# Kernel optimization log

Hardware: AMD Instinct MI355X
Metric: run time of the kernel (lower is better)

Reference implementation:

```python
import jax, jax.numpy as jnp
import numpy as np
import math

B, L, D, K = 16, 8192, 256, 320
BN_EPS = 1e-5


def setup_inputs() -> dict:
    key = jax.random.key(0)
    k1, k2, k3, k4 = jax.random.split(key, 4)
    x = jax.random.normal(k1, (B, L, D), dtype=jnp.float32)
    bn_weight = 1.0 + 0.1 * jax.random.normal(k2, (D,), dtype=jnp.float32)
    bn_bias = 0.1 * jax.random.normal(k3, (D,), dtype=jnp.float32)
    # xavier_uniform for Embedding(numCodes, codeDim)
    a = math.sqrt(6.0 / (K + D))
    codebook = jax.random.uniform(k4, (K, D), minval=-a, maxval=a, dtype=jnp.float32)
    return {"x": x, "bn_weight": bn_weight, "bn_bias": bn_bias, "codebook": codebook}


def batchnorm1d(x, weight, bias):
    # BatchNorm1d in training mode: stats over (batch, length) per channel,
    # biased variance for normalization (matches torch).
    mean = jnp.mean(x, axis=(0, 1))
    var = jnp.var(x, axis=(0, 1))
    return (x - mean) * jax.lax.rsqrt(var + BN_EPS) * weight + bias


def reference(x, bn_weight, bn_bias, codebook):
    xb = batchnorm1d(x, bn_weight, bn_bias)            # [B, L, D]
    flat = xb.reshape(-1, D)                           # [B*L, D]
    # squared euclidean distance (same argmin as torch.cdist)
    d2 = (jnp.sum(flat * flat, axis=-1, keepdims=True)
          - 2.0 * flat @ codebook.T
          + jnp.sum(codebook * codebook, axis=-1))     # [B*L, K]
    indices = jnp.argmin(d2, axis=-1)                  # [B*L]
    codes = codebook[indices].reshape(B, L, D)         # gather nearest codes
    return codes, indices.reshape(B, L, 1)
```

## Files before the change

### kernel.cpp

```cpp
#include <hip/hip_runtime.h>
#include <hip/hip_bf16.h>

#define NROW 131072
#define D 256
#define K 320
#define BN_EPS 1e-5f
#define FIXSCALE 16777216.0f

typedef _Float16 half8 __attribute__((ext_vector_type(8)));
typedef float f32x4 __attribute__((ext_vector_type(4)));


__global__ __launch_bounds__(256) void k_zero(unsigned long long* __restrict__ acc) {
  acc[threadIdx.x] = 0ull;
  acc[256 + threadIdx.x] = 0ull;
}

__global__ __launch_bounds__(256) void k_stats_partial(const float* __restrict__ x,
                                                       unsigned long long* __restrict__ acc) {
  const int d = threadIdx.x;
  const int blk = blockIdx.x;
  const float* p = x + (size_t)blk * 256 * D + d;
  float s = 0.f, q = 0.f;
  #pragma unroll 4
  for (int r = 0; r < 256; ++r) {
    float v = p[(size_t)r * D];
    s += v;
    q = fmaf(v, v, q);
  }
  long long si = llrintf(s * FIXSCALE);
  long long qi = llrintf(q * FIXSCALE);
  atomicAdd(&acc[d],       (unsigned long long)si);
  atomicAdd(&acc[256 + d], (unsigned long long)qi);
}

__global__ __launch_bounds__(256) void k_stats_final(const unsigned long long* __restrict__ acc,
                                                     const float* __restrict__ cb,
                                                     float* __restrict__ meanb,
                                                     float* __restrict__ rsb,
                                                     float* __restrict__ cnorm) {
  const int t = threadIdx.x;
  if (blockIdx.x == 0) {
    double s = (double)(long long)acc[t]       / (double)FIXSCALE;
    double q = (double)(long long)acc[256 + t] / (double)FIXSCALE;
    double mean = s / (double)NROW;
    double var  = q / (double)NROW - mean * mean;
    meanb[t] = (float)mean;
    rsb[t]   = (float)(1.0 / sqrt(var + (double)BN_EPS));
  } else {
    for (int code = t; code < K; code += 256) {
      const float* c = cb + (size_t)code * D;
      float s = 0.f;
      for (int dd = 0; dd < D; ++dd) s = fmaf(c[dd], c[dd], s);
      cnorm[code] = s;
    }
  }
}

__global__ __launch_bounds__(64) void k_cbprep(const float* __restrict__ cb,
                                               _Float16* __restrict__ cbx) {
  const int nt = blockIdx.x;
  const int ks = blockIdx.y;
  const int l  = threadIdx.x;
  const int code = nt * 16 + (l & 15);
  const int d0 = ks * 32 + (l >> 4) * 8;
  const float* src = cb + (size_t)code * D + d0;
  const size_t bh = ((size_t)(nt * 2 + 0) * 8 + ks) * 512 + l * 8;
  const size_t bl = ((size_t)(nt * 2 + 1) * 8 + ks) * 512 + l * 8;
  #pragma unroll
  for (int j = 0; j < 8; ++j) {
    float v = src[j];
    _Float16 h = (_Float16)v;
    _Float16 lo = (_Float16)(v - (float)h);
    cbx[bh + j] = h;
    cbx[bl + j] = lo;
  }
}

__global__ __launch_bounds__(512) void k_main(const float* __restrict__ x,
                                              const float* __restrict__ w,
                                              const float* __restrict__ bias,
                                              const float* __restrict__ cb,
                                              const float* __restrict__ meanb,
                                              const float* __restrict__ rsb,
                                              const float* __restrict__ cnorm,
                                              const _Float16* __restrict__ cbx,
                                              float* __restrict__ out) {
  __shared__ _Float16 Bbuf[2][16384];
  __shared__ float sxs[256];
  __shared__ int bsel[256];

  const int t = threadIdx.x;
  const int lane = t & 63;
  const int wv = t >> 6;
  const int c15 = lane & 15;
  const int g = lane >> 4;
  const int row0 = (int)blockIdx.x * 256;

  float4 s0, s1, s2, s3;
  const char* stg_src = (const char*)cbx + (size_t)t * 16;
#define ISSUE(c) {                                                  \
    const char* p_ = stg_src + (size_t)(c) * 32768;                 \
    s0 = *(const float4*)(p_);                                      \
    s1 = *(const float4*)(p_ + 8192);                               \
    s2 = *(const float4*)(p_ + 16384);                              \
    s3 = *(const float4*)(p_ + 24576);                              \
  }
#define WRITE(b) {                                                  \
    char* q_ = (char*)Bbuf[b] + t * 16;                             \
    *(float4*)(q_)         = s0;                                    \
    *(float4*)(q_ + 8192)  = s1;                                    \
    *(float4*)(q_ + 16384) = s2;                                    \
    *(float4*)(q_ + 24576) = s3;                                    \
  }

  ISSUE(0);

  half8 ah[2][8], al[2][8];
  float accq0 = 0.f, accq1 = 0.f;
  {
    const int dbase = g * 8;
    const float* xp0 = x + (size_t)(row0 + wv * 32 + c15) * D + dbase;
    const float* xp1 = x + (size_t)(row0 + wv * 32 + 16 + c15) * D + dbase;
    #pragma unroll
    for (int ks = 0; ks < 8; ++ks) {
      const int d0 = dbase + ks * 32;
      float4 m0 = *(const float4*)(meanb + d0);
      float4 m1 = *(const float4*)(meanb + d0 + 4);
      float4 r0 = *(const float4*)(rsb + d0);
      float4 r1 = *(const float4*)(rsb + d0 + 4);
      float4 w0 = *(const float4*)(w + d0);
      float4 w1 = *(const float4*)(w + d0 + 4);
      float4 b0 = *(const float4*)(bias + d0);
      float4 b1 = *(const float4*)(bias + d0 + 4);
      {
        float4 xa = *(const float4*)(xp0 + ks * 32);
        float4 xb2 = *(const float4*)(xp0 + ks * 32 + 4);
        float o0 = ((xa.x - m0.x) * r0.x) * w0.x + b0.x;
        float o1 = ((xa.y - m0.y) * r0.y) * w0.y + b0.y;
        float o2 = ((xa.z - m0.z) * r0.z) * w0.z + b0.z;
        float o3 = ((xa.w - m0.w) * r0.w) * w0.w + b0.w;
        float o4 = ((xb2.x - m1.x) * r1.x) * w1.x + b1.x;
        float o5 = ((xb2.y - m1.y) * r1.y) * w1.y + b1.y;
        float o6 = ((xb2.z - m1.z) * r1.z) * w1.z + b1.z;
        float o7 = ((xb2.w - m1.w) * r1.w) * w1.w + b1.w;
        accq0 = fmaf(o0, o0, accq0); accq0 = fmaf(o1, o1, accq0);
        accq0 = fmaf(o2, o2, accq0); accq0 = fmaf(o3, o3, accq0);
        accq0 = fmaf(o4, o4, accq0); accq0 = fmaf(o5, o5, accq0);
        accq0 = fmaf(o6, o6, accq0); accq0 = fmaf(o7, o7, accq0);
        _Float16 h;
        h = (_Float16)o0; ah[0][ks][0] = h; al[0][ks][0] = (_Float16)(o0 - (float)h);
        h = (_Float16)o1; ah[0][ks][1] = h; al[0][ks][1] = (_Float16)(o1 - (float)h);
        h = (_Float16)o2; ah[0][ks][2] = h; al[0][ks][2] = (_Float16)(o2 - (float)h);
        h = (_Float16)o3; ah[0][ks][3] = h; al[0][ks][3] = (_Float16)(o3 - (float)h);
        h = (_Float16)o4; ah[0][ks][4] = h; al[0][ks][4] = (_Float16)(o4 - (float)h);
        h = (_Float16)o5; ah[0][ks][5] = h; al[0][ks][5] = (_Float16)(o5 - (float)h);
        h = (_Float16)o6; ah[0][ks][6] = h; al[0][ks][6] = (_Float16)(o6 - (float)h);
        h = (_Float16)o7; ah[0][ks][7] = h; al[0][ks][7] = (_Float16)(o7 - (float)h);
      }
      {
        float4 xa = *(const float4*)(xp1 + ks * 32);
        float4 xb2 = *(const float4*)(xp1 + ks * 32 + 4);
        float o0 = ((xa.x - m0.x) * r0.x) * w0.x + b0.x;
        float o1 = ((xa.y - m0.y) * r0.y) * w0.y + b0.y;
        float o2 = ((xa.z - m0.z) * r0.z) * w0.z + b0.z;
        float o3 = ((xa.w - m0.w) * r0.w) * w0.w + b0.w;
        float o4 = ((xb2.x - m1.x) * r1.x) * w1.x + b1.x;
        float o5 = ((xb2.y - m1.y) * r1.y) * w1.y + b1.y;
        float o6 = ((xb2.z - m1.z) * r1.z) * w1.z + b1.z;
        float o7 = ((xb2.w - m1.w) * r1.w) * w1.w + b1.w;
        accq1 = fmaf(o0, o0, accq1); accq1 = fmaf(o1, o1, accq1);
        accq1 = fmaf(o2, o2, accq1); accq1 = fmaf(o3, o3, accq1);
        accq1 = fmaf(o4, o4, accq1); accq1 = fmaf(o5, o5, accq1);
        accq1 = fmaf(o6, o6, accq1); accq1 = fmaf(o7, o7, accq1);
        _Float16 h;
        h = (_Float16)o0; ah[1][ks][0] = h; al[1][ks][0] = (_Float16)(o0 - (float)h);
        h = (_Float16)o1; ah[1][ks][1] = h; al[1][ks][1] = (_Float16)(o1 - (float)h);
        h = (_Float16)o2; ah[1][ks][2] = h; al[1][ks][2] = (_Float16)(o2 - (float)h);
        h = (_Float16)o3; ah[1][ks][3] = h; al[1][ks][3] = (_Float16)(o3 - (float)h);
        h = (_Float16)o4; ah[1][ks][4] = h; al[1][ks][4] = (_Float16)(o4 - (float)h);
        h = (_Float16)o5; ah[1][ks][5] = h; al[1][ks][5] = (_Float16)(o5 - (float)h);
        h = (_Float16)o6; ah[1][ks][6] = h; al[1][ks][6] = (_Float16)(o6 - (float)h);
        h = (_Float16)o7; ah[1][ks][7] = h; al[1][ks][7] = (_Float16)(o7 - (float)h);
      }
    }
  }
  {
    float v0 = accq0 + __shfl_xor(accq0, 16);
    float sx0 = v0 + __shfl_xor(v0, 32);
    float v1 = accq1 + __shfl_xor(accq1, 16);
    float sx1 = v1 + __shfl_xor(v1, 32);
    if (lane < 16) {
      sxs[wv * 32 + lane]      = sx0;
      sxs[wv * 32 + 16 + lane] = sx1;
    }
  }

  WRITE(0);
  ISSUE(1);
  __syncthreads();

  float bv[2][4];
  int   bix[2][4];
  #pragma unroll
  for (int i = 0; i < 2; ++i)
    #pragma unroll
    for (int r = 0; r < 4; ++r) { bv[i][r] = 3.4e38f; bix[i][r] = 0x7fffffff; }

  float sxr[2][4];
  #pragma unroll
  for (int i = 0; i < 2; ++i)
    #pragma unroll
    for (int r = 0; r < 4; ++r) sxr[i][r] = sxs[wv * 32 + i * 16 + g * 4 + r];

  for (int c = 0; c < 10; ++c) {
    if (c + 1 < 10) WRITE((c + 1) & 1);
    if (c + 2 < 10) ISSUE(c + 2);

    const _Float16* bb = Bbuf[c & 1] + lane * 8;
    f32x4 acc[2][2];
    #pragma unroll
    for (int i = 0; i < 2; ++i)
      #pragma unroll
      for (int tt = 0; tt < 2; ++tt) acc[i][tt] = (f32x4){0.f, 0.f, 0.f, 0.f};

    #pragma unroll
    for (int tt = 0; tt < 2; ++tt) {
      #pragma unroll
      for (int ks = 0; ks < 8; ++ks) {
        half8 bh = *(const half8*)(bb + ((tt * 2 + 0) * 8 + ks) * 512);
        half8 bl = *(const half8*)(bb + ((tt * 2 + 1) * 8 + ks) * 512);
        #pragma unroll
        for (int i = 0; i < 2; ++i) {
          acc[i][tt] = __builtin_amdgcn_mfma_f32_16x16x32_f16(ah[i][ks], bh, acc[i][tt], 0, 0, 0);
          acc[i][tt] = __builtin_amdgcn_mfma_f32_16x16x32_f16(ah[i][ks], bl, acc[i][tt], 0, 0, 0);
          acc[i][tt] = __builtin_amdgcn_mfma_f32_16x16x32_f16(al[i][ks], bh, acc[i][tt], 0, 0, 0);
        }
      }
    }

    #pragma unroll
    for (int tt = 0; tt < 2; ++tt) {
      const int code = c * 32 + tt * 16 + c15;
      const float cn = cnorm[code];
      #pragma unroll
      for (int i = 0; i < 2; ++i) {
        #pragma unroll
        for (int r = 0; r < 4; ++r) {
          const float d2 = (sxr[i][r] - 2.0f * acc[i][tt][r]) + cn;
          if (d2 < bv[i][r] || (d2 == bv[i][r] && code < bix[i][r])) {
            bv[i][r] = d2; bix[i][r] = code;
          }
        }
      }
    }
    if (c < 9) __syncthreads();
  }

  #pragma unroll
  for (int off = 8; off >= 1; off >>= 1) {
    #pragma unroll
    for (int i = 0; i < 2; ++i)
      #pragma unroll
      for (int r = 0; r < 4; ++r) {
        const float ov = __shfl_xor(bv[i][r], off);
        const int   oi = __shfl_xor(bix[i][r], off);
        if (ov < bv[i][r] || (ov == bv[i][r] && oi < bix[i][r])) {
          bv[i][r] = ov; bix[i][r] = oi;
        }
      }
  }
  if (c15 == 0) {
    #pragma unroll
    for (int i = 0; i < 2; ++i)
      #pragma unroll
      for (int r = 0; r < 4; ++r) {
        const int row = wv * 32 + i * 16 + g * 4 + r;
        bsel[row] = bix[i][r];
        out[(size_t)NROW * D + row0 + row] = (float)bix[i][r];
      }
  }
  __syncthreads();

  {
    const int lr = t >> 1;
    const int q = t & 1;
    const int code = bsel[lr];
    const float* cp = cb + (size_t)code * D;
    float* op = out + (size_t)(row0 + lr) * D;
    #pragma unroll
    for (int e = 0; e < 16; ++e) {
      *(float4*)(op + (e * 2 + q) * 4) = *(const float4*)(cp + (e * 2 + q) * 4);
    }
  }
#undef ISSUE
#undef WRITE
}

extern "C" void kernel_launch(void* const* d_in, const int* in_sizes, int n_in,
                              void* d_out, int out_size, void* d_ws, size_t ws_size,
                              hipStream_t stream) {
  const float* x    = (const float*)d_in[0];
  const float* w    = (const float*)d_in[1];
  const float* bias = (const float*)d_in[2];
  const float* cb   = (const float*)d_in[3];
  float* out = (float*)d_out;

  unsigned long long* acc = (unsigned long long*)d_ws;
  float* meanb = (float*)((char*)d_ws + 4096);
  float* rsb   = meanb + 256;
  float* cnorm = rsb + 256;
  _Float16* cbx = (_Float16*)((char*)d_ws + 8192);

  k_zero<<<1, 256, 0, stream>>>(acc);
  k_cbprep<<<dim3(20, 8), 64, 0, stream>>>(cb, cbx);
  k_stats_partial<<<512, 256, 0, stream>>>(x, acc);
  k_stats_final<<<2, 256, 0, stream>>>(acc, cb, meanb, rsb, cnorm);
  k_main<<<NROW / 256, 512, 0, stream>>>(x, w, bias, cb, meanb, rsb, cnorm, cbx, out);
}
```

Before: 160.9 us.

## Shrink main kernel blocks to 128 rows and fold zeroing into cbprep

The main kernel goes from 512 threads covering 256 rows to 256 threads covering 128 rows. Each codebook chunk is now 16 codes instead of 32, so the loop runs 20 iterations and the LDS double buffer is halved. Smaller blocks, less shared memory and fewer live accumulators are meant to raise occupancy and give more blocks across the CUs, at the cost of reloading the codebook twice as often per row and twice as many barriers. The separate accumulator-zeroing kernel is folded into an extra block of the codebook-prep kernel, which removes one launch. The first staging write is also moved ahead of the row-norm shuffle reduction.

```diff
diff --git a/kernel.cpp b/kernel.cpp
--- a/kernel.cpp
+++ b/kernel.cpp
@@ -10,11 +10,6 @@
 typedef _Float16 half8 __attribute__((ext_vector_type(8)));
 typedef float f32x4 __attribute__((ext_vector_type(4)));
 
-
-__global__ __launch_bounds__(256) void k_zero(unsigned long long* __restrict__ acc) {
-  acc[threadIdx.x] = 0ull;
-  acc[256 + threadIdx.x] = 0ull;
-}
 
 __global__ __launch_bounds__(256) void k_stats_partial(const float* __restrict__ x,
                                                        unsigned long long* __restrict__ acc) {
@@ -58,10 +53,17 @@
 }
 
 __global__ __launch_bounds__(64) void k_cbprep(const float* __restrict__ cb,
-                                               _Float16* __restrict__ cbx) {
-  const int nt = blockIdx.x;
-  const int ks = blockIdx.y;
-  const int l  = threadIdx.x;
+                                               _Float16* __restrict__ cbx,
+                                               unsigned long long* __restrict__ acc) {
+  const int b = blockIdx.x;
+  const int l = threadIdx.x;
+  if (b == 160) {
+    #pragma unroll
+    for (int j = 0; j < 8; ++j) acc[j * 64 + l] = 0ull;
+    return;
+  }
+  const int nt = b >> 3;
+  const int ks = b & 7;
   const int code = nt * 16 + (l & 15);
   const int d0 = ks * 32 + (l >> 4) * 8;
   const float* src = cb + (size_t)code * D + d0;
@@ -77,7 +79,7 @@
   }
 }
 
-__global__ __launch_bounds__(512) void k_main(const float* __restrict__ x,
+__global__ __launch_bounds__(256) void k_main(const float* __restrict__ x,
                                               const float* __restrict__ w,
                                               const float* __restrict__ bias,
                                               const float* __restrict__ cb,
@@ -86,32 +88,32 @@
                                               const float* __restrict__ cnorm,
                                               const _Float16* __restrict__ cbx,
                                               float* __restrict__ out) {
-  __shared__ _Float16 Bbuf[2][16384];
-  __shared__ float sxs[256];
-  __shared__ int bsel[256];
+  __shared__ _Float16 Bbuf[2][8192];
+  __shared__ float sxs[128];
+  __shared__ int bsel[128];
 
   const int t = threadIdx.x;
   const int lane = t & 63;
   const int wv = t >> 6;
   const int c15 = lane & 15;
   const int g = lane >> 4;
-  const int row0 = (int)blockIdx.x * 256;
+  const int row0 = (int)blockIdx.x * 128;
 
   float4 s0, s1, s2, s3;
   const char* stg_src = (const char*)cbx + (size_t)t * 16;
 #define ISSUE(c) {                                                  \
-    const char* p_ = stg_src + (size_t)(c) * 32768;                 \
+    const char* p_ = stg_src + (size_t)(c) * 16384;                 \
     s0 = *(const float4*)(p_);                                      \
-    s1 = *(const float4*)(p_ + 8192);                               \
-    s2 = *(const float4*)(p_ + 16384);                              \
-    s3 = *(const float4*)(p_ + 24576);                              \
+    s1 = *(const float4*)(p_ + 4096);                               \
+    s2 = *(const float4*)(p_ + 8192);                               \
+    s3 = *(const float4*)(p_ + 12288);                              \
   }
 #define WRITE(b) {                                                  \
-    char* q_ = (char*)Bbuf[b] + t * 16;                             \
+    char* q_ = (char*)Bbuf[(b)] + t * 16;                           \
     *(float4*)(q_)         = s0;                                    \
-    *(float4*)(q_ + 8192)  = s1;                                    \
-    *(float4*)(q_ + 16384) = s2;                                    \
-    *(float4*)(q_ + 24576) = s3;                                    \
+    *(float4*)(q_ + 4096)  = s1;                                    \
+    *(float4*)(q_ + 8192)  = s2;                                    \
+    *(float4*)(q_ + 12288) = s3;                                    \
   }
 
   ISSUE(0);
@@ -185,6 +187,10 @@
       }
     }
   }
+
+  WRITE(0);
+  ISSUE(1);
+
   {
     float v0 = accq0 + __shfl_xor(accq0, 16);
     float sx0 = v0 + __shfl_xor(v0, 32);
@@ -195,9 +201,6 @@
       sxs[wv * 32 + 16 + lane] = sx1;
     }
   }
-
-  WRITE(0);
-  ISSUE(1);
   __syncthreads();
 
   float bv[2][4];
@@ -213,48 +216,40 @@
     #pragma unroll
     for (int r = 0; r < 4; ++r) sxr[i][r] = sxs[wv * 32 + i * 16 + g * 4 + r];
 
-  for (int c = 0; c < 10; ++c) {
-    if (c + 1 < 10) WRITE((c + 1) & 1);
-    if (c + 2 < 10) ISSUE(c + 2);
-
-    const _Float16* bb = Bbuf[c & 1] + lane * 8;
-    f32x4 acc[2][2];
-    #pragma unroll
-    for (int i = 0; i < 2; ++i)
-      #pragma unroll
-      for (int tt = 0; tt < 2; ++tt) acc[i][tt] = (f32x4){0.f, 0.f, 0.f, 0.f};
-
-    #pragma unroll
-    for (int tt = 0; tt < 2; ++tt) {
+  for (int c = 0; c < 20; ++c) {
+    if (c + 1 < 20) WRITE((c + 1) & 1);
+    if (c + 2 < 20) ISSUE(c + 2);
+
+    {
+      const _Float16* bb = Bbuf[c & 1] + lane * 8;
+      f32x4 acc0 = (f32x4){0.f, 0.f, 0.f, 0.f};
+      f32x4 acc1 = (f32x4){0.f, 0.f, 0.f, 0.f};
       #pragma unroll
       for (int ks = 0; ks < 8; ++ks) {
-        half8 bh = *(const half8*)(bb + ((tt * 2 + 0) * 8 + ks) * 512);
-        half8 bl = *(const half8*)(bb + ((tt * 2 + 1) * 8 + ks) * 512);
-        #pragma unroll
-        for (int i = 0; i < 2; ++i) {
-          acc[i][tt] = __builtin_amdgcn_mfma_f32_16x16x32_f16(ah[i][ks], bh, acc[i][tt], 0, 0, 0);
-          acc[i][tt] = __builtin_amdgcn_mfma_f32_16x16x32_f16(ah[i][ks], bl, acc[i][tt], 0, 0, 0);
-          acc[i][tt] = __builtin_amdgcn_mfma_f32_16x16x32_f16(al[i][ks], bh, acc[i][tt], 0, 0, 0);
-        }
-      }
-    }
-
-    #pragma unroll
-    for (int tt = 0; tt < 2; ++tt) {
-      const int code = c * 32 + tt * 16 + c15;
+        half8 bh = *(const half8*)(bb + ks * 512);
+        half8 bl = *(const half8*)(bb + 4096 + ks * 512);
+        acc0 = __builtin_amdgcn_mfma_f32_16x16x32_f16(ah[0][ks], bh, acc0, 0, 0, 0);
+        acc0 = __builtin_amdgcn_mfma_f32_16x16x32_f16(ah[0][ks], bl, acc0, 0, 0, 0);
+        acc0 = __builtin_amdgcn_mfma_f32_16x16x32_f16(al[0][ks], bh, acc0, 0, 0, 0);
+        acc1 = __builtin_amdgcn_mfma_f32_16x16x32_f16(ah[1][ks], bh, acc1, 0, 0, 0);
+        acc1 = __builtin_amdgcn_mfma_f32_16x16x32_f16(ah[1][ks], bl, acc1, 0, 0, 0);
+        acc1 = __builtin_amdgcn_mfma_f32_16x16x32_f16(al[1][ks], bh, acc1, 0, 0, 0);
+      }
+      const int code = c * 16 + c15;
       const float cn = cnorm[code];
       #pragma unroll
-      for (int i = 0; i < 2; ++i) {
-        #pragma unroll
-        for (int r = 0; r < 4; ++r) {
-          const float d2 = (sxr[i][r] - 2.0f * acc[i][tt][r]) + cn;
-          if (d2 < bv[i][r] || (d2 == bv[i][r] && code < bix[i][r])) {
-            bv[i][r] = d2; bix[i][r] = code;
-          }
+      for (int r = 0; r < 4; ++r) {
+        const float d20 = (sxr[0][r] - 2.0f * acc0[r]) + cn;
+        if (d20 < bv[0][r] || (d20 == bv[0][r] && code < bix[0][r])) {
+          bv[0][r] = d20; bix[0][r] = code;
         }
-      }
-    }
-    if (c < 9) __syncthreads();
+        const float d21 = (sxr[1][r] - 2.0f * acc1[r]) + cn;
+        if (d21 < bv[1][r] || (d21 == bv[1][r] && code < bix[1][r])) {
+          bv[1][r] = d21; bix[1][r] = code;
+        }
+      }
+    }
+    if (c < 19) __syncthreads();
   }
 
   #pragma unroll
@@ -289,7 +284,7 @@
     const float* cp = cb + (size_t)code * D;
     float* op = out + (size_t)(row0 + lr) * D;
     #pragma unroll
-    for (int e = 0; e < 16; ++e) {
+    for (int e = 0; e < 32; ++e) {
       *(float4*)(op + (e * 2 + q) * 4) = *(const float4*)(cp + (e * 2 + q) * 4);
     }
   }
@@ -312,9 +307,8 @@
   float* cnorm = rsb + 256;
   _Float16* cbx = (_Float16*)((char*)d_ws + 8192);
 
-  k_zero<<<1, 256, 0, stream>>>(acc);
-  k_cbprep<<<dim3(20, 8), 64, 0, stream>>>(cb, cbx);
+  k_cbprep<<<161, 64, 0, stream>>>(cb, cbx, acc);
   k_stats_partial<<<512, 256, 0, stream>>>(x, acc);
   k_stats_final<<<2, 256, 0, stream>>>(acc, cb, meanb, rsb, cnorm);
-  k_main<<<NROW / 256, 512, 0, stream>>>(x, w, bias, cb, meanb, rsb, cnorm, cbx, out);
-}
+  k_main<<<NROW / 128, 256, 0, stream>>>(x, w, bias, cb, meanb, rsb, cnorm, cbx, out);
+}
```

Result: slower. 165.7 us (+3.0%).
